# Kernel tuning notes

Measured on AMD Instinct MI355X. Metric: run time of the kernel, lower is better.

Reference implementation:

```python
import jax, jax.numpy as jnp
import numpy as np

TAU = 0.1            # tau_instance == tau_proto == tau_guidance
ALPHA_RES = 0.2
LOGIT_SCALE = 5.0
K_NEI = 5
N_WAYS = 20
N_SHOTS = 5


def l2n(x):
    return x / jnp.maximum(jnp.linalg.norm(x, axis=-1, keepdims=True), 1e-12)


def sparse_adj(f, k, tau):
    # sim: [B, n, n]; keep only top-k per row, softmax over them
    sim = jnp.einsum('bnd,bmd->bnm', f, f)
    vals, idx = jax.lax.top_k(sim, k)
    B, n, _ = sim.shape
    mask = jnp.full_like(sim, -jnp.inf)
    bi = jnp.arange(B)[:, None, None]
    ri = jnp.arange(n)[None, :, None]
    mask = mask.at[bi, ri, idx].set(vals)
    return jax.nn.softmax(mask / tau, axis=-1)


def gnn_layer(x, adj, W, b, s):
    # message passing + linear + tanh + scaled residual (dropout=0 / eval)
    msg = jnp.einsum('bnm,bmd->bnd', adj, x)
    upd = jnp.tanh(msg @ W.T + b)
    return x + s * upd


def setup_inputs() -> dict:
    key = jax.random.key(0)
    ks = jax.random.split(key, 10)
    B, N, K, Q, D, L = 256, N_WAYS, N_SHOTS, 75, 512, 4
    NT = N * K + Q
    xav = 1.0 / np.sqrt(D)
    return {
        'V_feat': jax.random.normal(ks[0], (B, NT, D), jnp.float32),
        'P_feat': jax.random.normal(ks[1], (B, N, D), jnp.float32),
        'query_y': jax.random.randint(ks[2], (B, Q), 0, N),
        'igb_W': jax.random.normal(ks[3], (L, D, D), jnp.float32) * xav,
        'igb_b': jnp.zeros((L, D), jnp.float32),
        'igb_scale': jax.random.normal(ks[4], (L,), jnp.float32) * 0.1,
        'pgb_W': jax.random.normal(ks[5], (L, D, D), jnp.float32) * xav,
        'pgb_b': jnp.zeros((L, D), jnp.float32),
        'pgb_scale': jax.random.normal(ks[6], (L,), jnp.float32) * 0.1,
        'alpha': jax.random.uniform(ks[7], (), jnp.float32),
        'beta': jax.random.uniform(ks[8], (), jnp.float32),
    }


def reference(V_feat, P_feat, query_y, igb_W, igb_b, igb_scale,
              pgb_W, pgb_b, pgb_scale, alpha, beta):
    B, NT, D = V_feat.shape
    N, K = N_WAYS, N_SHOTS
    NK = N * K
    Q = NT - NK
    L = igb_W.shape[0]

    V = l2n(V_feat)
    P = l2n(P_feat)
    V0, P0 = V, P

    yl = query_y.reshape(B * Q)
    total = jnp.float32(0.0)
    final_logits = None
    for i in range(L):
        # instance graph branch
        adj_I = sparse_adj(V, K_NEI, TAU)
        V = gnn_layer(V, adj_I, igb_W[i], igb_b[i], igb_scale[i])
        V = l2n((1.0 - ALPHA_RES) * V + ALPHA_RES * V0)
        # prototype graph branch
        adj_P = sparse_adj(P, min(K_NEI, N), TAU)
        P = gnn_layer(P, adj_P, pgb_W[i], pgb_b[i], pgb_scale[i])
        P = l2n((1.0 - ALPHA_RES) * P + ALPHA_RES * P0)
        # visual class centers and adapted prototypes
        VC = l2n(V[:, :NK, :].reshape(B, N, K, D).mean(axis=2))
        Pa = l2n(alpha * P + (1.0 - alpha) * VC)
        # cross-modal softmax guidance
        sims = jnp.einsum('bnd,bmd->bnm', V, Pa)
        soft = jax.nn.softmax(sims / TAU, axis=-1)
        guide = jnp.einsum('bnm,bmd->bnd', soft, Pa)
        V = l2n(beta * V + (1.0 - beta) * guide)
        # per-step logits and CE loss (label_smoothing = 0)
        logits = LOGIT_SCALE * jnp.einsum('bqd,bnd->bqn', V[:, NK:, :], Pa)
        lf = logits.reshape(B * Q, N)
        ce = jnp.mean(jax.nn.logsumexp(lf, axis=-1)
                      - jnp.take_along_axis(lf, yl[:, None], axis=1)[:, 0])
        total = total + ce
        final_logits = logits

    loss = total / L
    pred = jnp.argmax(final_logits.reshape(B * Q, N), axis=-1)
    acc = jnp.mean((pred == yl).astype(jnp.float32))
    return (loss, acc)
```

## Files before the change

kernel.cpp:

```cpp
#include <hip/hip_runtime.h>
#include <math.h>

#define B_EP 256
#define NT 175
#define NWAYS 20
#define KSHOT 5
#define NKS 100
#define NQ 75
#define DIM 512
#define NLAYERS 4
#define TAU_INV 10.0f
#define LOGIT_SCALE 5.0f
#define KNEI 5
#define SIMLD 176
#define STLD2 72
#define PALD 520
#define NVB 700

typedef unsigned int u32;
typedef unsigned short u16;
typedef __attribute__((ext_vector_type(8))) short s16x8;
typedef __attribute__((ext_vector_type(4))) float f32x4;

__device__ __forceinline__ float waveReduceSum(float v) {
#pragma unroll
  for (int off = 32; off >= 1; off >>= 1) v += __shfl_xor(v, off);
  return v;
}

__device__ __forceinline__ u32 pack2bf(float a, float b) {
  u32 ua = __float_as_uint(a), ub = __float_as_uint(b);
  ua = (ua + 0x7FFFu + ((ua >> 16) & 1u)) >> 16;
  ub = (ub + 0x7FFFu + ((ub >> 16) & 1u)) >> 16;
  return ua | (ub << 16);
}

__device__ __forceinline__ u16 pack1bf(float a) {
  u32 ua = __float_as_uint(a);
  return (u16)((ua + 0x7FFFu + ((ua >> 16) & 1u)) >> 16);
}

__device__ __forceinline__ float bflo(u32 u) { return __uint_as_float(u << 16); }
__device__ __forceinline__ float bfhi(u32 u) { return __uint_as_float(u & 0xFFFF0000u); }
__device__ __forceinline__ float bf1(u16 h) { return __uint_as_float((u32)h << 16); }

__device__ __forceinline__ float tanh_fast(float x) {
  float e = __expf(2.f * x);
  return 1.f - 2.f * __builtin_amdgcn_rcpf(e + 1.f);
}

__device__ __forceinline__ s16x8 ldfrag(const u16* p) {
  return __builtin_bit_cast(s16x8, *(const uint4*)p);
}

__device__ __forceinline__ void gload16(const u16* g, u16* l) {
  __builtin_amdgcn_global_load_lds(
      (const __attribute__((address_space(1))) void*)g,
      (__attribute__((address_space(3))) void*)l, 16, 0, 0);
}

__global__ void init_accum_kernel(float* acc) {
  if (threadIdx.x < 16) acc[threadIdx.x] = 0.f;
}

__global__ void cvt_bf16_kernel(const float* __restrict__ in,
                                u16* __restrict__ out, int n8) {
  int t = blockIdx.x * 256 + threadIdx.x;
  if (t >= n8) return;
  const float4* p = (const float4*)(in + (size_t)t * 8);
  float4 a = p[0], b = p[1];
  uint4 r;
  r.x = pack2bf(a.x, a.y);
  r.y = pack2bf(a.z, a.w);
  r.z = pack2bf(b.x, b.y);
  r.w = pack2bf(b.z, b.w);
  *(uint4*)(out + (size_t)t * 8) = r;
}

__global__ void l2n_init_kernel(const float* __restrict__ in,
                                u16* __restrict__ outb,
                                u16* __restrict__ out0b) {
  const size_t row = blockIdx.x;
  const int lane = threadIdx.x;
  const float* src = in + row * DIM;
  float4 a = *(const float4*)(src + 4 * lane);
  float4 b = *(const float4*)(src + 256 + 4 * lane);
  float ss = a.x * a.x + a.y * a.y + a.z * a.z + a.w * a.w +
             b.x * b.x + b.y * b.y + b.z * b.z + b.w * b.w;
  ss = waveReduceSum(ss);
  const float inv = 1.f / fmaxf(sqrtf(ss), 1e-12f);
  a.x *= inv; a.y *= inv; a.z *= inv; a.w *= inv;
  b.x *= inv; b.y *= inv; b.z *= inv; b.w *= inv;
  uint2 pa, pb;
  pa.x = pack2bf(a.x, a.y); pa.y = pack2bf(a.z, a.w);
  pb.x = pack2bf(b.x, b.y); pb.y = pack2bf(b.z, b.w);
  *(uint2*)(outb + row * DIM + 4 * lane) = pa;
  *(uint2*)(outb + row * DIM + 256 + 4 * lane) = pb;
  *(uint2*)(out0b + row * DIM + 4 * lane) = pa;
  *(uint2*)(out0b + row * DIM + 256 + 4 * lane) = pb;
}

__global__ __launch_bounds__(256) void sim_topk_msg_kernel(
    const u16* __restrict__ VB, u16* __restrict__ MSGB) {
  const int p = blockIdx.x;
  const int b = p & 255, sl = p >> 8;
  const int tid = threadIdx.x;
  const int wave = tid >> 6, lane = tid & 63;
  __shared__ __align__(16) u16 SIMs[64 * SIMLD];
  __shared__ __align__(16) u16 Vst[192 * STLD2];
  const u16* Vb = VB + (size_t)b * NT * DIM;
  for (int i = tid; i < (192 - NT) * STLD2; i += 256)
    Vst[NT * STLD2 + i] = 0;
  f32x4 acc[4][4];
#pragma unroll
  for (int m = 0; m < 4; ++m)
#pragma unroll
    for (int n = 0; n < 4; ++n) acc[m][n] = (f32x4){0.f, 0.f, 0.f, 0.f};
  const int part = lane >> 4;
  for (int kk = 0; kk < DIM; kk += 64) {
    __syncthreads();
#pragma unroll
    for (int r6 = 0; r6 < 6; ++r6) {
      const int idx = tid + 256 * r6;
      if (idx < NT * 8) {
        const int row = idx >> 3, pp = idx & 7;
        uint4 v = *(const uint4*)(Vb + (size_t)row * DIM + kk + pp * 8);
        *(uint4*)&Vst[row * STLD2 + pp * 8] = v;
      }
    }
    __syncthreads();
    if (wave < 3) {
#pragma unroll
      for (int ks = 0; ks < 2; ++ks) {
        s16x8 fa[4], fb[4];
#pragma unroll
        for (int m = 0; m < 4; ++m)
          fa[m] = ldfrag(&Vst[(sl * 64 + m * 16 + (lane & 15)) * STLD2 +
                              ks * 32 + part * 8]);
#pragma unroll
        for (int n = 0; n < 4; ++n)
          fb[n] = ldfrag(&Vst[(wave * 64 + n * 16 + (lane & 15)) * STLD2 +
                              ks * 32 + part * 8]);
#pragma unroll
        for (int m = 0; m < 4; ++m)
#pragma unroll
          for (int n = 0; n < 4; ++n)
            acc[m][n] = __builtin_amdgcn_mfma_f32_16x16x32_bf16(
                fa[m], fb[n], acc[m][n], 0, 0, 0);
      }
    }
  }
  const int r_ = (lane >> 4) * 4, c_ = lane & 15;
  if (wave < 3) {
#pragma unroll
    for (int m = 0; m < 4; ++m)
#pragma unroll
      for (int n = 0; n < 4; ++n)
#pragma unroll
        for (int j = 0; j < 4; ++j) {
          const int rl = m * 16 + r_ + j;
          const int c = wave * 64 + n * 16 + c_;
          if (sl * 64 + rl < NT && c < NT)
            SIMs[rl * SIMLD + c] = pack1bf(acc[m][n][j]);
        }
  }
  __syncthreads();
  for (int rl = wave; rl < 64; rl += 4) {
    const int rg = sl * 64 + rl;
    if (rg >= NT) break;
    u32 pk[3];
#pragma unroll
    for (int t = 0; t < 3; ++t) {
      int j = lane + 64 * t;
      if (j < NT) {
        u32 v = SIMs[rl * SIMLD + j];
        u32 key = v ^ ((v >> 15) ? 0xFFFFu : 0x8000u);
        pk[t] = (key << 8) | (u32)(255 - j);
      } else {
        pk[t] = 0u;
      }
    }
    float topv[KNEI];
    int topi[KNEI];
#pragma unroll
    for (int t = 0; t < KNEI; ++t) {
      u32 c = max(pk[0], max(pk[1], pk[2]));
#pragma unroll
      for (int off = 32; off >= 1; off >>= 1)
        c = max(c, (u32)__shfl_xor((int)c, off));
#pragma unroll
      for (int u = 0; u < 3; ++u)
        if (pk[u] == c) pk[u] = 0u;
      const u32 k16 = (c >> 8) & 0xFFFFu;
      const u32 v16 = (k16 & 0x8000u) ? (k16 ^ 0x8000u) : (~k16 & 0xFFFFu);
      topv[t] = bf1((u16)v16);
      topi[t] = 255 - (int)(c & 0xFFu);
    }
    float w[KNEI];
    float wsum = 0.f;
#pragma unroll
    for (int t = 0; t < KNEI; ++t) {
      w[t] = __expf((topv[t] - topv[0]) * TAU_INV);
      wsum += w[t];
    }
    const float invs = 1.f / wsum;
    float a8[8] = {0.f, 0.f, 0.f, 0.f, 0.f, 0.f, 0.f, 0.f};
#pragma unroll
    for (int t = 0; t < KNEI; ++t) {
      uint4 v = *(const uint4*)(Vb + (size_t)topi[t] * DIM + 8 * lane);
      a8[0] += w[t] * bflo(v.x); a8[1] += w[t] * bfhi(v.x);
      a8[2] += w[t] * bflo(v.y); a8[3] += w[t] * bfhi(v.y);
      a8[4] += w[t] * bflo(v.z); a8[5] += w[t] * bfhi(v.z);
      a8[6] += w[t] * bflo(v.w); a8[7] += w[t] * bfhi(v.w);
    }
    uint4 r;
    r.x = pack2bf(a8[0] * invs, a8[1] * invs);
    r.y = pack2bf(a8[2] * invs, a8[3] * invs);
    r.z = pack2bf(a8[4] * invs, a8[5] * invs);
    r.w = pack2bf(a8[6] * invs, a8[7] * invs);
    *(uint4*)(MSGB + ((size_t)b * NT + rg) * DIM + 8 * lane) = r;
  }
}

__global__ __launch_bounds__(512) void gemm_fused_kernel(
    const u16* __restrict__ Av, const u16* __restrict__ Ap,
    const u16* __restrict__ Wv, const u16* __restrict__ Wp,
    const float* __restrict__ bias_v, const float* __restrict__ bias_p,
    const float* __restrict__ sv, const float* __restrict__ sp,
    u16* __restrict__ XBv, u16* __restrict__ XBp,
    const u16* __restrict__ X0v, const u16* __restrict__ X0p) {
  const int bid = blockIdx.x;
  const bool isV = bid < NVB;
  const int row0 = (isV ? bid : bid - NVB) * 64;
  const u16* A = isV ? Av : Ap;
  const u16* W = isV ? Wv : Wp;
  const float* bias = isV ? bias_v : bias_p;
  const float* scale_ptr = isV ? sv : sp;
  u16* XB = isV ? XBv : XBp;
  const u16* X0B = isV ? X0v : X0p;
  const int tid = threadIdx.x, wave = tid >> 6, lane = tid & 63;
  __shared__ __align__(16) u16 smem[18432];
  u16* Bs = smem;
  u16* As = smem + 16384;
  f32x4 acc[4][4];
#pragma unroll
  for (int m = 0; m < 4; ++m)
#pragma unroll
    for (int n = 0; n < 4; ++n) acc[m][n] = (f32x4){0.f, 0.f, 0.f, 0.f};
  const int rsrc = lane >> 2;
  const int ksrc = (lane & 3) * 8;
  for (int kk = 0; kk < DIM; kk += 32) {
#pragma unroll
    for (int q = 0; q < 4; ++q) {
      const int t = wave * 4 + q;
      gload16(W + (size_t)(t * 16 + rsrc) * DIM + kk + ksrc, Bs + t * 512);
    }
    if (wave < 4)
      gload16(A + (size_t)(row0 + wave * 16 + rsrc) * DIM + kk + ksrc,
              As + wave * 512);
    __syncthreads();
    s16x8 fa[4], fb[4];
#pragma unroll
    for (int m = 0; m < 4; ++m)
      fa[m] = ldfrag(&As[(m * 16 + (lane & 15)) * 32 + (lane >> 4) * 8]);
#pragma unroll
    for (int n = 0; n < 4; ++n)
      fb[n] = ldfrag(
          &Bs[(wave * 64 + n * 16 + (lane & 15)) * 32 + (lane >> 4) * 8]);
#pragma unroll
    for (int m = 0; m < 4; ++m)
#pragma unroll
      for (int n = 0; n < 4; ++n)
        acc[m][n] = __builtin_amdgcn_mfma_f32_16x16x32_bf16(fa[m], fb[n],
                                                            acc[m][n], 0, 0, 0);
    __syncthreads();
  }
  const float s = *scale_ptr;
  const int rq = lane >> 4, c_ = lane & 15;
  const int prow = tid >> 4, sub = tid & 15;
  const int rq2 = ((prow >> 2) & 3) << 1;
#pragma unroll
  for (int half = 0; half < 2; ++half) {
    __syncthreads();
#pragma unroll
    for (int n = 0; n < 4; ++n) {
      const int col = wave * 64 + n * 16 + c_;
      const float bc = bias[col];
      const int cbase = col >> 3, wof = col & 7;
#pragma unroll
      for (int mm = 0; mm < 2; ++mm) {
        const int m = half * 2 + mm;
#pragma unroll
        for (int j = 0; j < 4; ++j) {
          const int lr = mm * 16 + rq * 4 + j;
          const int cS = cbase ^ (((lr >> 2) & 3) << 1);
          smem[lr * 512 + cS * 8 + wof] =
              pack1bf(s * tanh_fast(acc[m][n][j] + bc));
        }
      }
    }
    __syncthreads();
    const int grow = row0 + half * 32 + prow;
    const u16* xrow = XB + (size_t)grow * DIM;
    const u16* x0row = X0B + (size_t)grow * DIM;
    float ss = 0.f;
#pragma unroll
    for (int i = 0; i < 4; ++i) {
      const int c = sub + 16 * i;
      uint4 xb = *(const uint4*)(xrow + c * 8);
      uint4 x0 = *(const uint4*)(x0row + c * 8);
      uint4 uu = *(const uint4*)&smem[prow * 512 + (c ^ rq2) * 8];
      float t0 = 0.8f * (bflo(xb.x) + bflo(uu.x)) + 0.2f * bflo(x0.x);
      float t1 = 0.8f * (bfhi(xb.x) + bfhi(uu.x)) + 0.2f * bfhi(x0.x);
      float t2 = 0.8f * (bflo(xb.y) + bflo(uu.y)) + 0.2f * bflo(x0.y);
      float t3 = 0.8f * (bfhi(xb.y) + bfhi(uu.y)) + 0.2f * bfhi(x0.y);
      float t4 = 0.8f * (bflo(xb.z) + bflo(uu.z)) + 0.2f * bflo(x0.z);
      float t5 = 0.8f * (bfhi(xb.z) + bfhi(uu.z)) + 0.2f * bfhi(x0.z);
      float t6 = 0.8f * (bflo(xb.w) + bflo(uu.w)) + 0.2f * bflo(x0.w);
      float t7 = 0.8f * (bfhi(xb.w) + bfhi(uu.w)) + 0.2f * bfhi(x0.w);
      ss += t0 * t0 + t1 * t1 + t2 * t2 + t3 * t3 + t4 * t4 + t5 * t5 +
            t6 * t6 + t7 * t7;
      uint4 tp;
      tp.x = pack2bf(t0, t1); tp.y = pack2bf(t2, t3);
      tp.z = pack2bf(t4, t5); tp.w = pack2bf(t6, t7);
      *(uint4*)&smem[prow * 512 + (c ^ rq2) * 8] = tp;
    }
#pragma unroll
    for (int off = 8; off >= 1; off >>= 1) ss += __shfl_xor(ss, off, 16);
    const float inv = 1.f / fmaxf(sqrtf(ss), 1e-12f);
    u16* orow = XB + (size_t)grow * DIM;
#pragma unroll
    for (int i = 0; i < 4; ++i) {
      const int c = sub + 16 * i;
      uint4 tp = *(const uint4*)&smem[prow * 512 + (c ^ rq2) * 8];
      uint4 r;
      r.x = pack2bf(bflo(tp.x) * inv, bfhi(tp.x) * inv);
      r.y = pack2bf(bflo(tp.y) * inv, bfhi(tp.y) * inv);
      r.z = pack2bf(bflo(tp.z) * inv, bfhi(tp.z) * inv);
      r.w = pack2bf(bflo(tp.w) * inv, bfhi(tp.w) * inv);
      *(uint4*)(orow + c * 8) = r;
    }
  }
}

__global__ __launch_bounds__(64) void p_branch_kernel(
    const u16* __restrict__ PB, u16* __restrict__ PMSGB) {
  const int b = blockIdx.x;
  const int lane = threadIdx.x;
  __shared__ __align__(16) u16 Pl[32][520];
  __shared__ float Gl[NWAYS][NWAYS];
  __shared__ float Wl[NWAYS][KNEI];
  __shared__ int Il[NWAYS][KNEI];
  const u16* Pb = PB + (size_t)b * NWAYS * DIM;
  for (int c = lane; c < 32 * 64; c += 64) {
    int m = c >> 6, ko = (c & 63) * 8;
    uint4 v = {0, 0, 0, 0};
    if (m < NWAYS) v = *(const uint4*)(Pb + (size_t)m * DIM + ko);
    *(uint4*)&Pl[m][ko] = v;
  }
  __syncthreads();
  f32x4 acc[2][2];
#pragma unroll
  for (int m = 0; m < 2; ++m)
#pragma unroll
    for (int n = 0; n < 2; ++n) acc[m][n] = (f32x4){0.f, 0.f, 0.f, 0.f};
  for (int kk = 0; kk < DIM; kk += 32) {
    s16x8 f[2];
#pragma unroll
    for (int m = 0; m < 2; ++m)
      f[m] = ldfrag(&Pl[m * 16 + (lane & 15)][kk + (lane >> 4) * 8]);
#pragma unroll
    for (int m = 0; m < 2; ++m)
#pragma unroll
      for (int n = 0; n < 2; ++n)
        acc[m][n] = __builtin_amdgcn_mfma_f32_16x16x32_bf16(f[m], f[n],
                                                            acc[m][n], 0, 0, 0);
  }
  const int r_ = (lane >> 4) * 4, c_ = lane & 15;
#pragma unroll
  for (int m = 0; m < 2; ++m)
#pragma unroll
    for (int n = 0; n < 2; ++n)
#pragma unroll
      for (int j = 0; j < 4; ++j) {
        int r = m * 16 + r_ + j, c = n * 16 + c_;
        if (r < NWAYS && c < NWAYS) Gl[r][c] = acc[m][n][j];
      }
  __syncthreads();
  if (lane < NWAYS) {
    float sims[NWAYS];
#pragma unroll
    for (int m = 0; m < NWAYS; ++m) sims[m] = Gl[lane][m];
    float topv[KNEI];
    int topi[KNEI];
#pragma unroll
    for (int t = 0; t < KNEI; ++t) {
      float bv = -INFINITY;
      int bi = 0;
#pragma unroll
      for (int m = 0; m < NWAYS; ++m)
        if (sims[m] > bv) { bv = sims[m]; bi = m; }
      sims[bi] = -INFINITY;
      topv[t] = bv;
      topi[t] = bi;
    }
    float w[KNEI], wsum = 0.f;
#pragma unroll
    for (int t = 0; t < KNEI; ++t) {
      w[t] = __expf((topv[t] - topv[0]) * TAU_INV);
      wsum += w[t];
    }
    const float invs = 1.f / wsum;
#pragma unroll
    for (int t = 0; t < KNEI; ++t) {
      Wl[lane][t] = w[t] * invs;
      Il[lane][t] = topi[t];
    }
  }
  __syncthreads();
  u16* outp = PMSGB + (size_t)b * NWAYS * DIM;
#pragma unroll 4
  for (int n = 0; n < NWAYS; ++n) {
    float a8[8] = {0.f, 0.f, 0.f, 0.f, 0.f, 0.f, 0.f, 0.f};
#pragma unroll
    for (int t = 0; t < KNEI; ++t) {
      const float w = Wl[n][t];
      uint4 v = *(const uint4*)&Pl[Il[n][t]][8 * lane];
      a8[0] += w * bflo(v.x); a8[1] += w * bfhi(v.x);
      a8[2] += w * bflo(v.y); a8[3] += w * bfhi(v.y);
      a8[4] += w * bflo(v.z); a8[5] += w * bfhi(v.z);
      a8[6] += w * bflo(v.w); a8[7] += w * bfhi(v.w);
    }
    uint4 r;
    r.x = pack2bf(a8[0], a8[1]);
    r.y = pack2bf(a8[2], a8[3]);
    r.z = pack2bf(a8[4], a8[5]);
    r.w = pack2bf(a8[6], a8[7]);
    *(uint4*)(outp + (size_t)n * DIM + 8 * lane) = r;
  }
}

__global__ void vcpa_kernel(const u16* __restrict__ VB,
                            const u16* __restrict__ PB,
                            const float* __restrict__ alpha_ptr,
                            u16* __restrict__ PAB) {
  const int row = blockIdx.x;
  const int bb = row / NWAYS, n = row - bb * NWAYS;
  const int lane = threadIdx.x;
  const u16* base = VB + ((size_t)bb * NT + (size_t)n * KSHOT) * DIM;
  float a8[8] = {0.f, 0.f, 0.f, 0.f, 0.f, 0.f, 0.f, 0.f};
#pragma unroll
  for (int k = 0; k < KSHOT; ++k) {
    uint2 x0 = *(const uint2*)(base + (size_t)k * DIM + 4 * lane);
    uint2 x1 = *(const uint2*)(base + (size_t)k * DIM + 256 + 4 * lane);
    a8[0] += bflo(x0.x); a8[1] += bfhi(x0.x);
    a8[2] += bflo(x0.y); a8[3] += bfhi(x0.y);
    a8[4] += bflo(x1.x); a8[5] += bfhi(x1.x);
    a8[6] += bflo(x1.y); a8[7] += bfhi(x1.y);
  }
  float ss = 0.f;
#pragma unroll
  for (int t = 0; t < 8; ++t) ss += a8[t] * a8[t];
  ss = waveReduceSum(ss);
  const float inv = 1.f / fmaxf(sqrtf(ss), 1e-12f);
#pragma unroll
  for (int t = 0; t < 8; ++t) a8[t] *= inv;
  const float alpha = *alpha_ptr, oma = 1.f - alpha;
  {
    uint2 p0 = *(const uint2*)(PB + (size_t)row * DIM + 4 * lane);
    uint2 p1 = *(const uint2*)(PB + (size_t)row * DIM + 256 + 4 * lane);
    a8[0] = alpha * bflo(p0.x) + oma * a8[0];
    a8[1] = alpha * bfhi(p0.x) + oma * a8[1];
    a8[2] = alpha * bflo(p0.y) + oma * a8[2];
    a8[3] = alpha * bfhi(p0.y) + oma * a8[3];
    a8[4] = alpha * bflo(p1.x) + oma * a8[4];
    a8[5] = alpha * bfhi(p1.x) + oma * a8[5];
    a8[6] = alpha * bflo(p1.y) + oma * a8[6];
    a8[7] = alpha * bfhi(p1.y) + oma * a8[7];
  }
  float s2 = 0.f;
#pragma unroll
  for (int t = 0; t < 8; ++t) s2 += a8[t] * a8[t];
  s2 = waveReduceSum(s2);
  const float inv2 = 1.f / fmaxf(sqrtf(s2), 1e-12f);
  uint2 pa, pb;
  pa.x = pack2bf(a8[0] * inv2, a8[1] * inv2);
  pa.y = pack2bf(a8[2] * inv2, a8[3] * inv2);
  pb.x = pack2bf(a8[4] * inv2, a8[5] * inv2);
  pb.y = pack2bf(a8[6] * inv2, a8[7] * inv2);
  *(uint2*)(PAB + (size_t)row * DIM + 4 * lane) = pa;
  *(uint2*)(PAB + (size_t)row * DIM + 256 + 4 * lane) = pb;
}

__global__ __launch_bounds__(64) void sims_kernel(const u16* __restrict__ VB,
                                                  const u16* __restrict__ PAB,
                                                  float* __restrict__ SIMS,
                                                  float* __restrict__ G) {
  const int it = blockIdx.x, b = blockIdx.y;
  const int lane = threadIdx.x;
  __shared__ __align__(16) u16 As[64][32];
  __shared__ __align__(16) u16 Bs[32][32];
  const u16* Vb = VB + (size_t)b * NT * DIM;
  const u16* Pb = PAB + (size_t)b * NWAYS * DIM;
  f32x4 acc[4][2];
#pragma unroll
  for (int m = 0; m < 4; ++m)
#pragma unroll
    for (int n = 0; n < 2; ++n) acc[m][n] = (f32x4){0.f, 0.f, 0.f, 0.f};
  const int ra = it * 64 + lane;
  const int rb = lane & 31, kb = (lane >> 5) * 16;
  for (int kk = 0; kk < DIM; kk += 32) {
    if (ra < NT) {
      const uint4* g = (const uint4*)(Vb + (size_t)ra * DIM + kk);
#pragma unroll
      for (int q = 0; q < 4; ++q) *(uint4*)&As[lane][8 * q] = g[q];
    } else if (ra < NT + NWAYS) {
      const uint4* g = (const uint4*)(Pb + (size_t)(ra - NT) * DIM + kk);
#pragma unroll
      for (int q = 0; q < 4; ++q) *(uint4*)&As[lane][8 * q] = g[q];
    } else {
      uint4 z = {0, 0, 0, 0};
#pragma unroll
      for (int q = 0; q < 4; ++q) *(uint4*)&As[lane][8 * q] = z;
    }
    if (rb < NWAYS) {
      const uint4* g = (const uint4*)(Pb + (size_t)rb * DIM + kk + kb);
      *(uint4*)&Bs[rb][kb] = g[0];
      *(uint4*)&Bs[rb][kb + 8] = g[1];
    } else {
      uint4 z = {0, 0, 0, 0};
      *(uint4*)&Bs[rb][kb] = z;
      *(uint4*)&Bs[rb][kb + 8] = z;
    }
    __syncthreads();
    s16x8 fa[4], fb[2];
#pragma unroll
    for (int m = 0; m < 4; ++m)
      fa[m] = ldfrag(&As[m * 16 + (lane & 15)][(lane >> 4) * 8]);
#pragma unroll
    for (int n = 0; n < 2; ++n)
      fb[n] = ldfrag(&Bs[n * 16 + (lane & 15)][(lane >> 4) * 8]);
#pragma unroll
    for (int m = 0; m < 4; ++m)
#pragma unroll
      for (int n = 0; n < 2; ++n)
        acc[m][n] = __builtin_amdgcn_mfma_f32_16x16x32_bf16(fa[m], fb[n],
                                                            acc[m][n], 0, 0, 0);
    __syncthreads();
  }
  const int r_ = (lane >> 4) * 4, c_ = lane & 15;
#pragma unroll
  for (int m = 0; m < 4; ++m)
#pragma unroll
    for (int n = 0; n < 2; ++n)
#pragma unroll
      for (int j = 0; j < 4; ++j) {
        int r = it * 64 + m * 16 + r_ + j, c = n * 16 + c_;
        if (c >= NWAYS) continue;
        if (r < NT)
          SIMS[((size_t)b * NT + r) * NWAYS + c] = acc[m][n][j];
        else if (r < NT + NWAYS)
          G[(size_t)b * 400 + (r - NT) * NWAYS + c] = acc[m][n][j];
      }
}

__global__ __launch_bounds__(512) void tail2_kernel(
    u16* __restrict__ VB, const u16* __restrict__ PAB,
    const float* __restrict__ SIMS, const float* __restrict__ G,
    const int* __restrict__ qy, const float* __restrict__ beta_ptr,
    float* __restrict__ accum, int is_last) {
  const int b = blockIdx.x;
  const int tid = threadIdx.x, wave = tid >> 6, lane = tid & 63;
  __shared__ __align__(16) u16 palds[NWAYS * PALD];
  __shared__ float Gl[NWAYS][NWAYS + 1];
  __shared__ float red[16];
  for (int c = tid; c < NWAYS * 64; c += 512) {
    int m = c >> 6, ko = (c & 63) * 8;
    *(uint4*)&palds[m * PALD + ko] =
        *(const uint4*)(PAB + ((size_t)b * NWAYS + m) * DIM + ko);
  }
  for (int c = tid; c < NWAYS * NWAYS; c += 512)
    Gl[c / NWAYS][c % NWAYS] = G[(size_t)b * 400 + c];
  __syncthreads();
  const float beta = *beta_ptr, omb = 1.f - beta;
  float ce_acc = 0.f, ac_acc = 0.f;
  for (int row = wave; row < NT; row += 8) {
    const float* srow = SIMS + ((size_t)b * NT + row) * NWAYS;
    float s[NWAYS];
#pragma unroll
    for (int m = 0; m < NWAYS; ++m) s[m] = srow[m];
    float mx = s[0];
#pragma unroll
    for (int m = 1; m < NWAYS; ++m) mx = fmaxf(mx, s[m]);
    float e[NWAYS], wsum = 0.f, dN = 0.f;
#pragma unroll
    for (int m = 0; m < NWAYS; ++m) {
      e[m] = __expf((s[m] - mx) * TAU_INV);
      wsum += e[m];
      dN += e[m] * s[m];
    }
    const float cg = omb / wsum;
    const int ln = lane & 31;
    float sg = 0.f;
    if (ln < NWAYS) {
#pragma unroll
      for (int m = 0; m < NWAYS; ++m) sg += e[m] * Gl[m][ln];
    }
    float ege = (ln < NWAYS) ? e[ln] * sg : 0.f;
#pragma unroll
    for (int off = 16; off >= 1; off >>= 1) ege += __shfl_xor(ege, off, 32);
    const float nn2 = beta * beta + 2.f * beta * cg * dN + cg * cg * ege;
    const float inv = 1.f / fmaxf(sqrtf(nn2), 1e-12f);
    u16* vrow = VB + ((size_t)b * NT + row) * DIM;
    uint4 v4 = *(const uint4*)(vrow + 8 * lane);
    float t0 = 0.f, t1 = 0.f, t2 = 0.f, t3 = 0.f;
    float t4 = 0.f, t5 = 0.f, t6 = 0.f, t7 = 0.f;
#pragma unroll
    for (int m = 0; m < NWAYS; ++m) {
      uint4 p = *(const uint4*)&palds[m * PALD + 8 * lane];
      t0 += e[m] * bflo(p.x); t1 += e[m] * bfhi(p.x);
      t2 += e[m] * bflo(p.y); t3 += e[m] * bfhi(p.y);
      t4 += e[m] * bflo(p.z); t5 += e[m] * bfhi(p.z);
      t6 += e[m] * bflo(p.w); t7 += e[m] * bfhi(p.w);
    }
    uint4 r;
    r.x = pack2bf((beta * bflo(v4.x) + cg * t0) * inv,
                  (beta * bfhi(v4.x) + cg * t1) * inv);
    r.y = pack2bf((beta * bflo(v4.y) + cg * t2) * inv,
                  (beta * bfhi(v4.y) + cg * t3) * inv);
    r.z = pack2bf((beta * bflo(v4.z) + cg * t4) * inv,
                  (beta * bfhi(v4.z) + cg * t5) * inv);
    r.w = pack2bf((beta * bflo(v4.w) + cg * t6) * inv,
                  (beta * bfhi(v4.w) + cg * t7) * inv);
    *(uint4*)(vrow + 8 * lane) = r;
    if (row >= NKS) {
      float l = (ln < NWAYS)
                    ? LOGIT_SCALE * inv * (beta * s[ln] + cg * sg)
                    : -1e30f;
      float bv = l;
      int bi = ln;
#pragma unroll
      for (int off = 16; off >= 1; off >>= 1) {
        float ov = __shfl_xor(bv, off, 32);
        int oi = __shfl_xor(bi, off, 32);
        if (ov > bv || (ov == bv && oi < bi)) { bv = ov; bi = oi; }
      }
      float se = (ln < NWAYS) ? __expf(l - bv) : 0.f;
#pragma unroll
      for (int off = 16; off >= 1; off >>= 1) se += __shfl_xor(se, off, 32);
      const int yt = qy[b * NQ + (row - NKS)];
      const float ly = __shfl(l, yt, 32);
      if (lane == 0) {
        ce_acc += bv + __logf(se) - ly;
        ac_acc += (bi == yt) ? 1.f : 0.f;
      }
    }
  }
  if (lane == 0) {
    red[wave] = ce_acc;
    red[8 + wave] = ac_acc;
  }
  __syncthreads();
  if (tid == 0) {
    float ce = 0.f, ac = 0.f;
#pragma unroll
    for (int w8 = 0; w8 < 8; ++w8) {
      ce += red[w8];
      ac += red[8 + w8];
    }
    atomicAdd(&accum[0], ce);
    if (is_last) atomicAdd(&accum[1], ac);
  }
}

__global__ void finalize_kernel(const float* __restrict__ acc,
                                float* __restrict__ out) {
  out[0] = acc[0] / (float)(NLAYERS * B_EP * NQ);
  out[1] = acc[1] / (float)(B_EP * NQ);
}

extern "C" void kernel_launch(void* const* d_in, const int* in_sizes, int n_in,
                              void* d_out, int out_size, void* d_ws,
                              size_t ws_size, hipStream_t stream) {
  const float* V_feat = (const float*)d_in[0];
  const float* P_feat = (const float*)d_in[1];
  const int* query_y = (const int*)d_in[2];
  const float* igb_W = (const float*)d_in[3];
  const float* igb_b = (const float*)d_in[4];
  const float* igb_s = (const float*)d_in[5];
  const float* pgb_W = (const float*)d_in[6];
  const float* pgb_b = (const float*)d_in[7];
  const float* pgb_s = (const float*)d_in[8];
  const float* alpha = (const float*)d_in[9];
  const float* beta = (const float*)d_in[10];
  float* out = (float*)d_out;

  float* ws = (float*)d_ws;
  const size_t vsz = (size_t)B_EP * NT * DIM;
  const size_t psz = (size_t)B_EP * NWAYS * DIM;
  const size_t wsz = (size_t)NLAYERS * DIM * DIM;
  float* ACC = ws;
  float* SIMS = ws + 16;
  float* G = SIMS + (size_t)B_EP * NT * NWAYS;
  u16* VB = (u16*)(G + (size_t)B_EP * 400);
  u16* V0B = VB + vsz;
  u16* MSGB = V0B + vsz;
  u16* PB = MSGB + vsz;
  u16* P0B = PB + psz;
  u16* PMSGB = P0B + psz;
  u16* PAB = PMSGB + psz;
  u16* WB = PAB + psz;
  u16* WPB = WB + wsz;

  init_accum_kernel<<<1, 64, 0, stream>>>(ACC);
  l2n_init_kernel<<<B_EP * NT, 64, 0, stream>>>(V_feat, VB, V0B);
  l2n_init_kernel<<<B_EP * NWAYS, 64, 0, stream>>>(P_feat, PB, P0B);
  cvt_bf16_kernel<<<(int)(wsz / 8 / 256), 256, 0, stream>>>(igb_W, WB,
                                                            (int)(wsz / 8));
  cvt_bf16_kernel<<<(int)(wsz / 8 / 256), 256, 0, stream>>>(pgb_W, WPB,
                                                            (int)(wsz / 8));

  for (int i = 0; i < NLAYERS; ++i) {
    sim_topk_msg_kernel<<<3 * B_EP, 256, 0, stream>>>(VB, MSGB);
    p_branch_kernel<<<B_EP, 64, 0, stream>>>(PB, PMSGB);
    gemm_fused_kernel<<<NVB + B_EP * NWAYS / 64, 512, 0, stream>>>(
        MSGB, PMSGB, WB + (size_t)i * DIM * DIM, WPB + (size_t)i * DIM * DIM,
        igb_b + (size_t)i * DIM, pgb_b + (size_t)i * DIM, igb_s + i, pgb_s + i,
        VB, PB, V0B, P0B);

    vcpa_kernel<<<B_EP * NWAYS, 64, 0, stream>>>(VB, PB, alpha, PAB);
    sims_kernel<<<dim3(4, B_EP), 64, 0, stream>>>(VB, PAB, SIMS, G);
    tail2_kernel<<<B_EP, 512, 0, stream>>>(VB, PAB, SIMS, G, query_y, beta,
                                           ACC, (i == NLAYERS - 1) ? 1 : 0);
  }
  finalize_kernel<<<1, 1, 0, stream>>>(ACC, out);
}
```

Baseline: 930.2 us.

## Fuse prototype adaptation, similarity GEMM and tail into one episode kernel

Replaces the separate vcpa, sims and tail2 kernels with one per-episode kernel. It computes the adapted prototypes into shared memory, runs the V·Pa and Pa·Pa products with MFMA per wave, and keeps the similarity and Gram matrices in LDS before the softmax/guidance/loss stage. This removes two launches per layer and the global round trips for PAB, SIMS and G. In exchange, each episode is handled by a single 512-thread block, which lowers parallelism for the GEMM part and raises LDS use per block.

Measured after the change: 840.1 us. 9.7% less time.

```diff
diff --git a/kernel.cpp b/kernel.cpp
--- a/kernel.cpp
+++ b/kernel.cpp
@@ -15,6 +15,7 @@
 #define SIMLD 176
 #define STLD2 72
 #define PALD 520
+#define ASTLD 40
 #define NVB 700
 
 typedef unsigned int u32;
@@ -440,155 +441,126 @@
   }
 }
 
-__global__ void vcpa_kernel(const u16* __restrict__ VB,
-                            const u16* __restrict__ PB,
-                            const float* __restrict__ alpha_ptr,
-                            u16* __restrict__ PAB) {
-  const int row = blockIdx.x;
-  const int bb = row / NWAYS, n = row - bb * NWAYS;
-  const int lane = threadIdx.x;
-  const u16* base = VB + ((size_t)bb * NT + (size_t)n * KSHOT) * DIM;
-  float a8[8] = {0.f, 0.f, 0.f, 0.f, 0.f, 0.f, 0.f, 0.f};
-#pragma unroll
-  for (int k = 0; k < KSHOT; ++k) {
-    uint2 x0 = *(const uint2*)(base + (size_t)k * DIM + 4 * lane);
-    uint2 x1 = *(const uint2*)(base + (size_t)k * DIM + 256 + 4 * lane);
-    a8[0] += bflo(x0.x); a8[1] += bfhi(x0.x);
-    a8[2] += bflo(x0.y); a8[3] += bfhi(x0.y);
-    a8[4] += bflo(x1.x); a8[5] += bfhi(x1.x);
-    a8[6] += bflo(x1.y); a8[7] += bfhi(x1.y);
-  }
-  float ss = 0.f;
-#pragma unroll
-  for (int t = 0; t < 8; ++t) ss += a8[t] * a8[t];
-  ss = waveReduceSum(ss);
-  const float inv = 1.f / fmaxf(sqrtf(ss), 1e-12f);
-#pragma unroll
-  for (int t = 0; t < 8; ++t) a8[t] *= inv;
-  const float alpha = *alpha_ptr, oma = 1.f - alpha;
-  {
-    uint2 p0 = *(const uint2*)(PB + (size_t)row * DIM + 4 * lane);
-    uint2 p1 = *(const uint2*)(PB + (size_t)row * DIM + 256 + 4 * lane);
-    a8[0] = alpha * bflo(p0.x) + oma * a8[0];
-    a8[1] = alpha * bfhi(p0.x) + oma * a8[1];
-    a8[2] = alpha * bflo(p0.y) + oma * a8[2];
-    a8[3] = alpha * bfhi(p0.y) + oma * a8[3];
-    a8[4] = alpha * bflo(p1.x) + oma * a8[4];
-    a8[5] = alpha * bfhi(p1.x) + oma * a8[5];
-    a8[6] = alpha * bflo(p1.y) + oma * a8[6];
-    a8[7] = alpha * bfhi(p1.y) + oma * a8[7];
-  }
-  float s2 = 0.f;
-#pragma unroll
-  for (int t = 0; t < 8; ++t) s2 += a8[t] * a8[t];
-  s2 = waveReduceSum(s2);
-  const float inv2 = 1.f / fmaxf(sqrtf(s2), 1e-12f);
-  uint2 pa, pb;
-  pa.x = pack2bf(a8[0] * inv2, a8[1] * inv2);
-  pa.y = pack2bf(a8[2] * inv2, a8[3] * inv2);
-  pb.x = pack2bf(a8[4] * inv2, a8[5] * inv2);
-  pb.y = pack2bf(a8[6] * inv2, a8[7] * inv2);
-  *(uint2*)(PAB + (size_t)row * DIM + 4 * lane) = pa;
-  *(uint2*)(PAB + (size_t)row * DIM + 256 + 4 * lane) = pb;
-}
-
-__global__ __launch_bounds__(64) void sims_kernel(const u16* __restrict__ VB,
-                                                  const u16* __restrict__ PAB,
-                                                  float* __restrict__ SIMS,
-                                                  float* __restrict__ G) {
-  const int it = blockIdx.x, b = blockIdx.y;
-  const int lane = threadIdx.x;
-  __shared__ __align__(16) u16 As[64][32];
-  __shared__ __align__(16) u16 Bs[32][32];
-  const u16* Vb = VB + (size_t)b * NT * DIM;
-  const u16* Pb = PAB + (size_t)b * NWAYS * DIM;
-  f32x4 acc[4][2];
-#pragma unroll
-  for (int m = 0; m < 4; ++m)
-#pragma unroll
-    for (int n = 0; n < 2; ++n) acc[m][n] = (f32x4){0.f, 0.f, 0.f, 0.f};
-  const int ra = it * 64 + lane;
-  const int rb = lane & 31, kb = (lane >> 5) * 16;
-  for (int kk = 0; kk < DIM; kk += 32) {
-    if (ra < NT) {
-      const uint4* g = (const uint4*)(Vb + (size_t)ra * DIM + kk);
-#pragma unroll
-      for (int q = 0; q < 4; ++q) *(uint4*)&As[lane][8 * q] = g[q];
-    } else if (ra < NT + NWAYS) {
-      const uint4* g = (const uint4*)(Pb + (size_t)(ra - NT) * DIM + kk);
-#pragma unroll
-      for (int q = 0; q < 4; ++q) *(uint4*)&As[lane][8 * q] = g[q];
-    } else {
-      uint4 z = {0, 0, 0, 0};
-#pragma unroll
-      for (int q = 0; q < 4; ++q) *(uint4*)&As[lane][8 * q] = z;
-    }
-    if (rb < NWAYS) {
-      const uint4* g = (const uint4*)(Pb + (size_t)rb * DIM + kk + kb);
-      *(uint4*)&Bs[rb][kb] = g[0];
-      *(uint4*)&Bs[rb][kb + 8] = g[1];
-    } else {
-      uint4 z = {0, 0, 0, 0};
-      *(uint4*)&Bs[rb][kb] = z;
-      *(uint4*)&Bs[rb][kb + 8] = z;
-    }
-    __syncthreads();
-    s16x8 fa[4], fb[2];
-#pragma unroll
-    for (int m = 0; m < 4; ++m)
-      fa[m] = ldfrag(&As[m * 16 + (lane & 15)][(lane >> 4) * 8]);
-#pragma unroll
-    for (int n = 0; n < 2; ++n)
-      fb[n] = ldfrag(&Bs[n * 16 + (lane & 15)][(lane >> 4) * 8]);
-#pragma unroll
-    for (int m = 0; m < 4; ++m)
-#pragma unroll
-      for (int n = 0; n < 2; ++n)
-        acc[m][n] = __builtin_amdgcn_mfma_f32_16x16x32_bf16(fa[m], fb[n],
-                                                            acc[m][n], 0, 0, 0);
-    __syncthreads();
-  }
-  const int r_ = (lane >> 4) * 4, c_ = lane & 15;
-#pragma unroll
-  for (int m = 0; m < 4; ++m)
-#pragma unroll
-    for (int n = 0; n < 2; ++n)
-#pragma unroll
-      for (int j = 0; j < 4; ++j) {
-        int r = it * 64 + m * 16 + r_ + j, c = n * 16 + c_;
-        if (c >= NWAYS) continue;
-        if (r < NT)
-          SIMS[((size_t)b * NT + r) * NWAYS + c] = acc[m][n][j];
-        else if (r < NT + NWAYS)
-          G[(size_t)b * 400 + (r - NT) * NWAYS + c] = acc[m][n][j];
-      }
-}
-
-__global__ __launch_bounds__(512) void tail2_kernel(
-    u16* __restrict__ VB, const u16* __restrict__ PAB,
-    const float* __restrict__ SIMS, const float* __restrict__ G,
-    const int* __restrict__ qy, const float* __restrict__ beta_ptr,
-    float* __restrict__ accum, int is_last) {
+__global__ __launch_bounds__(512) void episode_post_kernel(
+    u16* __restrict__ VB, const u16* __restrict__ PB,
+    const int* __restrict__ qy, const float* __restrict__ alpha_ptr,
+    const float* __restrict__ beta_ptr, float* __restrict__ accum,
+    int is_last) {
   const int b = blockIdx.x;
   const int tid = threadIdx.x, wave = tid >> 6, lane = tid & 63;
   __shared__ __align__(16) u16 palds[NWAYS * PALD];
+  __shared__ __align__(16) u16 AstAll[7 * 32 * ASTLD];
+  __shared__ float SIMSl[NT * NWAYS];
   __shared__ float Gl[NWAYS][NWAYS + 1];
   __shared__ float red[16];
-  for (int c = tid; c < NWAYS * 64; c += 512) {
-    int m = c >> 6, ko = (c & 63) * 8;
-    *(uint4*)&palds[m * PALD + ko] =
-        *(const uint4*)(PAB + ((size_t)b * NWAYS + m) * DIM + ko);
-  }
-  for (int c = tid; c < NWAYS * NWAYS; c += 512)
-    Gl[c / NWAYS][c % NWAYS] = G[(size_t)b * 400 + c];
+  const u16* Vb0 = VB + (size_t)b * NT * DIM;
+  const float alpha = *alpha_ptr, oma = 1.f - alpha;
+  const float beta = *beta_ptr, omb = 1.f - beta;
+  for (int n = wave; n < NWAYS; n += 8) {
+    const u16* base = Vb0 + (size_t)n * KSHOT * DIM;
+    float a8[8] = {0.f, 0.f, 0.f, 0.f, 0.f, 0.f, 0.f, 0.f};
+#pragma unroll
+    for (int k = 0; k < KSHOT; ++k) {
+      uint4 v = *(const uint4*)(base + (size_t)k * DIM + 8 * lane);
+      a8[0] += bflo(v.x); a8[1] += bfhi(v.x);
+      a8[2] += bflo(v.y); a8[3] += bfhi(v.y);
+      a8[4] += bflo(v.z); a8[5] += bfhi(v.z);
+      a8[6] += bflo(v.w); a8[7] += bfhi(v.w);
+    }
+    float ss = 0.f;
+#pragma unroll
+    for (int t = 0; t < 8; ++t) ss += a8[t] * a8[t];
+    ss = waveReduceSum(ss);
+    const float inv = 1.f / fmaxf(sqrtf(ss), 1e-12f);
+    {
+      uint4 p = *(const uint4*)(PB + ((size_t)b * NWAYS + n) * DIM + 8 * lane);
+      a8[0] = alpha * bflo(p.x) + oma * a8[0] * inv;
+      a8[1] = alpha * bfhi(p.x) + oma * a8[1] * inv;
+      a8[2] = alpha * bflo(p.y) + oma * a8[2] * inv;
+      a8[3] = alpha * bfhi(p.y) + oma * a8[3] * inv;
+      a8[4] = alpha * bflo(p.z) + oma * a8[4] * inv;
+      a8[5] = alpha * bfhi(p.z) + oma * a8[5] * inv;
+      a8[6] = alpha * bflo(p.w) + oma * a8[6] * inv;
+      a8[7] = alpha * bfhi(p.w) + oma * a8[7] * inv;
+    }
+    float s2 = 0.f;
+#pragma unroll
+    for (int t = 0; t < 8; ++t) s2 += a8[t] * a8[t];
+    s2 = waveReduceSum(s2);
+    const float inv2 = 1.f / fmaxf(sqrtf(s2), 1e-12f);
+    uint4 r;
+    r.x = pack2bf(a8[0] * inv2, a8[1] * inv2);
+    r.y = pack2bf(a8[2] * inv2, a8[3] * inv2);
+    r.z = pack2bf(a8[4] * inv2, a8[5] * inv2);
+    r.w = pack2bf(a8[6] * inv2, a8[7] * inv2);
+    *(uint4*)&palds[n * PALD + 8 * lane] = r;
+  }
   __syncthreads();
-  const float beta = *beta_ptr, omb = 1.f - beta;
+  if (wave < 7) {
+    u16* Ast = AstAll + wave * (32 * ASTLD);
+    const int r0w = wave * 32;
+    f32x4 sacc[2][2];
+#pragma unroll
+    for (int m = 0; m < 2; ++m)
+#pragma unroll
+      for (int n = 0; n < 2; ++n) sacc[m][n] = (f32x4){0.f, 0.f, 0.f, 0.f};
+    const int part = lane >> 4, fr = lane & 15;
+    for (int kk = 0; kk < DIM; kk += 32) {
+      if (r0w < NT) {
+#pragma unroll
+        for (int q2 = 0; q2 < 2; ++q2) {
+          const int q = lane + 64 * q2;
+          const int r = q >> 2, pp = q & 3;
+          uint4 v =
+              *(const uint4*)(Vb0 + (size_t)(r0w + r) * DIM + kk + pp * 8);
+          *(uint4*)&Ast[r * ASTLD + pp * 8] = v;
+        }
+      }
+      s16x8 fa[2], fb[2];
+#pragma unroll
+      for (int m = 0; m < 2; ++m) {
+        const int row = r0w + m * 16 + fr;
+        const u16* ap;
+        if (row < NT) {
+          ap = &Ast[(m * 16 + fr) * ASTLD + part * 8];
+        } else {
+          int pr = row - NT;
+          if (pr > NWAYS - 1) pr = NWAYS - 1;
+          ap = &palds[pr * PALD + kk + part * 8];
+        }
+        fa[m] = ldfrag(ap);
+      }
+#pragma unroll
+      for (int n = 0; n < 2; ++n)
+        fb[n] = ldfrag(&palds[(n * 16 + fr) * PALD + kk + part * 8]);
+#pragma unroll
+      for (int m = 0; m < 2; ++m)
+#pragma unroll
+        for (int n = 0; n < 2; ++n)
+          sacc[m][n] = __builtin_amdgcn_mfma_f32_16x16x32_bf16(
+              fa[m], fb[n], sacc[m][n], 0, 0, 0);
+    }
+    const int r_ = (lane >> 4) * 4, c_ = lane & 15;
+#pragma unroll
+    for (int m = 0; m < 2; ++m)
+#pragma unroll
+      for (int n = 0; n < 2; ++n)
+#pragma unroll
+        for (int j = 0; j < 4; ++j) {
+          const int r = r0w + m * 16 + r_ + j, c = n * 16 + c_;
+          if (c >= NWAYS) continue;
+          if (r < NT)
+            SIMSl[r * NWAYS + c] = sacc[m][n][j];
+          else if (r < NT + NWAYS)
+            Gl[r - NT][c] = sacc[m][n][j];
+        }
+  }
+  __syncthreads();
   float ce_acc = 0.f, ac_acc = 0.f;
   for (int row = wave; row < NT; row += 8) {
-    const float* srow = SIMS + ((size_t)b * NT + row) * NWAYS;
     float s[NWAYS];
 #pragma unroll
-    for (int m = 0; m < NWAYS; ++m) s[m] = srow[m];
+    for (int m = 0; m < NWAYS; ++m) s[m] = SIMSl[row * NWAYS + m];
     float mx = s[0];
 #pragma unroll
     for (int m = 1; m < NWAYS; ++m) mx = fmaxf(mx, s[m]);
@@ -700,16 +672,13 @@
   const size_t psz = (size_t)B_EP * NWAYS * DIM;
   const size_t wsz = (size_t)NLAYERS * DIM * DIM;
   float* ACC = ws;
-  float* SIMS = ws + 16;
-  float* G = SIMS + (size_t)B_EP * NT * NWAYS;
-  u16* VB = (u16*)(G + (size_t)B_EP * 400);
+  u16* VB = (u16*)(ws + 16);
   u16* V0B = VB + vsz;
   u16* MSGB = V0B + vsz;
   u16* PB = MSGB + vsz;
   u16* P0B = PB + psz;
   u16* PMSGB = P0B + psz;
-  u16* PAB = PMSGB + psz;
-  u16* WB = PAB + psz;
+  u16* WB = PMSGB + psz;
   u16* WPB = WB + wsz;
 
   init_accum_kernel<<<1, 64, 0, stream>>>(ACC);
@@ -727,11 +696,8 @@
         MSGB, PMSGB, WB + (size_t)i * DIM * DIM, WPB + (size_t)i * DIM * DIM,
         igb_b + (size_t)i * DIM, pgb_b + (size_t)i * DIM, igb_s + i, pgb_s + i,
         VB, PB, V0B, P0B);
-
-    vcpa_kernel<<<B_EP * NWAYS, 64, 0, stream>>>(VB, PB, alpha, PAB);
-    sims_kernel<<<dim3(4, B_EP), 64, 0, stream>>>(VB, PAB, SIMS, G);
-    tail2_kernel<<<B_EP, 512, 0, stream>>>(VB, PAB, SIMS, G, query_y, beta,
-                                           ACC, (i == NLAYERS - 1) ? 1 : 0);
+    episode_post_kernel<<<B_EP, 512, 0, stream>>>(
+        VB, PB, query_y, alpha, beta, ACC, (i == NLAYERS - 1) ? 1 : 0);
   }
   finalize_kernel<<<1, 1, 0, stream>>>(ACC, out);
 }
```
